# Kernel tuning notes

Measured on AMD Instinct MI355X. Metric: run time of the kernel, lower is better.

## Reference

```python
import jax, jax.numpy as jnp
import numpy as np
from jax import lax

DIM = 64           # LHMSA dim
C3 = 3 * DIM       # high-band channels
HEADS = C3 // 32   # 6
WS = 8             # window size
SHIFT = 4          # shift size
EPS = 1e-6


def _ln_chw(x, w, b):
    # channel-last layer norm applied to BCHW input over C
    xt = x.transpose(0, 2, 3, 1)
    mu = xt.mean(-1, keepdims=True)
    var = ((xt - mu) ** 2).mean(-1, keepdims=True)
    y = (xt - mu) / jnp.sqrt(var + EPS) * w + b
    return y.transpose(0, 3, 1, 2)


def _conv1x1(x, w):
    # w: (out_c, in_c), no bias
    return jnp.einsum('bchw,oc->bohw', x, w)


def _dwconv3(x, w):
    # depthwise 3x3, w: (C,1,3,3)
    C = x.shape[1]
    return lax.conv_general_dilated(x, w, (1, 1), ((1, 1), (1, 1)),
                                    dimension_numbers=('NCHW', 'OIHW', 'NCHW'),
                                    feature_group_count=C)


def _gelu(x):
    return jax.nn.gelu(x, approximate=False)


def _dwt(x):
    x01 = x[:, :, 0::2, :] * 0.5
    x02 = x[:, :, 1::2, :] * 0.5
    x1 = x01[:, :, :, 0::2]; x2 = x02[:, :, :, 0::2]
    x3 = x01[:, :, :, 1::2]; x4 = x02[:, :, :, 1::2]
    ll = x1 + x2 + x3 + x4
    high = jnp.concatenate([-x1 - x2 + x3 + x4,
                            -x1 + x2 - x3 + x4,
                            x1 - x2 - x3 + x4], axis=1)
    return ll, high


def _iwt(ll, high):
    B, C, H, W = ll.shape
    hl, lh, hh = jnp.split(high, 3, axis=1)
    x1 = (ll - hl - lh + hh) * 0.5
    x2 = (ll - hl + lh - hh) * 0.5
    x3 = (ll + hl - lh - hh) * 0.5
    x4 = (ll + hl + lh + hh) * 0.5
    even = jnp.stack([x1, x3], axis=-1).reshape(B, C, H, 2 * W)  # rows 0::2
    odd = jnp.stack([x2, x4], axis=-1).reshape(B, C, H, 2 * W)   # rows 1::2
    return jnp.stack([even, odd], axis=-2).reshape(B, C, 2 * H, 2 * W)


def _swin_mhsa(x, qkv_w, qkv_b, proj_w, proj_b, rpb_table, rpi):
    # x: (B, C3, H, W); H,W divisible by WS -> no padding path
    B, C, H, W = x.shape
    dh = C // HEADS
    scale = dh ** (-0.5)
    xh = x.transpose(0, 2, 3, 1)                           # BHWC
    xh = jnp.roll(xh, (-SHIFT, -SHIFT), axis=(1, 2))
    nh, nw = H // WS, W // WS
    xw = xh.reshape(B, nh, WS, nw, WS, C).transpose(0, 1, 3, 2, 4, 5)
    xw = xw.reshape(B * nh * nw, WS * WS, C)               # (nW, N, C)
    qkv = xw @ qkv_w.T + qkv_b                             # (nW, N, 3C)
    qkv = qkv.reshape(-1, WS * WS, 3, HEADS, dh).transpose(2, 0, 3, 1, 4)
    q, k, v = qkv[0], qkv[1], qkv[2]                       # (nW, h, N, dh)
    attn = jnp.einsum('whnd,whmd->whnm', q, k) * scale
    bias = rpb_table[rpi.reshape(-1)].reshape(WS * WS, WS * WS, HEADS)
    attn = jax.nn.softmax(attn + bias.transpose(2, 0, 1)[None], axis=-1)
    out = jnp.einsum('whnm,whmd->whnd', attn, v)
    out = out.transpose(0, 2, 1, 3).reshape(-1, WS * WS, C)
    out = out.reshape(B, nh, nw, WS, WS, C).transpose(0, 1, 3, 2, 4, 5)
    out = out.reshape(B, H, W, C)
    out = jnp.roll(out, (SHIFT, SHIFT), axis=(1, 2))
    out = out @ proj_w.T + proj_b
    return out.transpose(0, 3, 1, 2)


def _rel_pos_index():
    coords = np.stack(np.meshgrid(np.arange(WS), np.arange(WS), indexing='ij'))
    cf = coords.reshape(2, -1)
    rel = (cf[:, :, None] - cf[:, None, :]).transpose(1, 2, 0).astype(np.int64)
    rel[:, :, 0] += WS - 1
    rel[:, :, 1] += WS - 1
    rel[:, :, 0] *= 2 * WS - 1
    return rel.sum(-1)


def setup_inputs() -> dict:
    key = jax.random.key(0)
    ks = jax.random.split(key, 12)
    B, H, W = 2, 512, 512
    x = jax.random.normal(ks[0], (B, DIM, H, W), jnp.float32)
    s = 0.02
    inp = {
        'x': x,
        'norm_w': jnp.ones((C3,), jnp.float32),
        'norm_b': jnp.zeros((C3,), jnp.float32),
        'qkv_w': jax.random.normal(ks[1], (3 * C3, C3), jnp.float32) * s,
        'qkv_b': jnp.zeros((3 * C3,), jnp.float32),
        'proj_w': jax.random.normal(ks[2], (C3, C3), jnp.float32) * s,
        'proj_b': jnp.zeros((C3,), jnp.float32),
        'rpb_table': jax.random.normal(ks[3], ((2 * WS - 1) ** 2, HEADS), jnp.float32) * s,
        'aux_dw_w': jax.random.normal(ks[4], (DIM, 1, 3, 3), jnp.float32) * 0.1,
        'aux_pw_w': jax.random.normal(ks[5], (DIM, DIM), jnp.float32) * s,
        'cg1_w': jax.random.normal(ks[6], (C3 * 3 // 12, DIM), jnp.float32) * s,
        'cg2_w': jax.random.normal(ks[7], (C3, C3 * 3 // 12), jnp.float32) * s,
        'po_w': jax.random.normal(ks[8], (DIM, DIM), jnp.float32) * s,
        'gamma_main': jnp.full((1,), 1e-4, jnp.float32),
        'gamma_aux': jnp.full((1,), 0.5, jnp.float32),
        'gamma_cross': jnp.full((1,), 1e-5, jnp.float32),
        'rel_pos_index': jnp.asarray(_rel_pos_index(), jnp.int32),
    }
    return inp


def reference(x, norm_w, norm_b, qkv_w, qkv_b, proj_w, proj_b, rpb_table,
              aux_dw_w, aux_pw_w, cg1_w, cg2_w, po_w,
              gamma_main, gamma_aux, gamma_cross, rel_pos_index):
    ll, high = _dwt(x)
    high_norm = _ln_chw(high, norm_w, norm_b)
    refined_high = high + gamma_main * _swin_mhsa(high_norm, qkv_w, qkv_b,
                                                  proj_w, proj_b, rpb_table,
                                                  rel_pos_index)
    refined_ll = ll + gamma_aux * _conv1x1(_gelu(_dwconv3(ll, aux_dw_w)), aux_pw_w)
    gap = ll.mean((2, 3), keepdims=True)
    cross = jax.nn.sigmoid(_conv1x1(_gelu(_conv1x1(gap, cg1_w)), cg2_w))
    refined_high = refined_high * (1.0 + gamma_cross * (cross - 0.5) * 2.0)
    out = _iwt(refined_ll, refined_high)
    return _conv1x1(out - x, po_w)
```

## Files before the change

kernel.cpp:

```cpp
#include <hip/hip_runtime.h>
#include <hip/hip_bf16.h>
#include <math.h>

typedef __hip_bfloat16 bf16;
typedef short s8v __attribute__((ext_vector_type(8)));
typedef float f4v __attribute__((ext_vector_type(4)));
#define MFMA16(a,b,c) __builtin_amdgcn_mfma_f32_16x16x32_bf16(a,b,c,0,0,0)

#define B2   2
#define C64  64
#define C3   192
#define HEADS 6
#define NWIN 2048

#define P_NORMW 0
#define P_NORMB 192
#define P_QKVW  384
#define P_QKVB  110976
#define P_PROJW 111552
#define P_PROJB 148416
#define P_RPB   148608
#define P_AUXDW 149958
#define P_AUXPW 150534
#define P_CG1   154630
#define P_CG2   157702
#define P_PO    166918
#define P_GM    171014
#define P_GA    171015
#define P_GC    171016

#define WS_FLAG   0
#define WS_PARAMS 256
#define WS_GAP    684544
#define WS_AMUL   685568
#define WS_CVAL   687616
#define WS_TSTAT  689664
#define WS_LL     1738240
#define WS_DLLW   18515456
#define WS_WOUT   35292672
#define WS_HRAW   85624320
#define WS_WQKV   135955968
#define WS_WPROJ  136177152
#define WS_WPW    136250880
#define WS_WPO    136259072
#define WS_S12    136267264
#define WS_BIAS6  136271872

__device__ __forceinline__ float bfu(unsigned short u){
  return __uint_as_float(((unsigned)u) << 16);
}
__device__ __forceinline__ float LDR(const void* p, long i, bool isf){
  return isf ? ((const float*)p)[i] : bfu(((const unsigned short*)p)[i]);
}
template<bool ISF>
__device__ __forceinline__ float4 LD4(const void* p, long i){
  if constexpr (ISF) return *(const float4*)((const float*)p + i);
  else {
    const ushort4 u = *(const ushort4*)((const bf16*)p + i);
    float4 r; r.x = bfu(u.x); r.y = bfu(u.y); r.z = bfu(u.z); r.w = bfu(u.w);
    return r;
  }
}
template<bool ISF>
__device__ __forceinline__ void ST(void* p, long i, float v){
  if constexpr (ISF) ((float*)p)[i] = v;
  else ((bf16*)p)[i] = __float2bfloat16(v);
}
__device__ __forceinline__ float gelu_f(float x){
  const float z = 0.7978845608028654f * (x + 0.044715f * x*x*x);
  const float t = 1.f - 2.f / (__expf(2.f*z) + 1.f);
  return 0.5f * x * (1.f + t);
}
__device__ __forceinline__ unsigned pk2(float a, float b){
  return (unsigned)__bfloat16_as_ushort(__float2bfloat16(a)) |
         ((unsigned)__bfloat16_as_ushort(__float2bfloat16(b)) << 16);
}
__device__ __forceinline__ uint4 pk8(const float* v){
  uint4 r;
  r.x = pk2(v[0], v[1]); r.y = pk2(v[2], v[3]);
  r.z = pk2(v[4], v[5]); r.w = pk2(v[6], v[7]);
  return r;
}
__device__ __forceinline__ void gld16(const void* g, void* l){
  __builtin_amdgcn_global_load_lds(
      (const __attribute__((address_space(1))) void*)g,
      (__attribute__((address_space(3))) void*)l, 16, 0, 0);
}

__global__ __launch_bounds__(256) void detect_kernel(const void* x, int* flag){
  __shared__ int wildcnt;
  if (threadIdx.x == 0) wildcnt = 0;
  __syncthreads();
  const unsigned short* u = (const unsigned short*)x;
  int wild = 0;
  for (int i = threadIdx.x; i < 2048; i += 256){
    unsigned int v = ((unsigned int)u[i]) << 16;
    float f = __uint_as_float(v);
    float a = fabsf(f);
    if (!(a < 1e8f) || (a > 0.f && a < 1e-8f)) wild++;
  }
  atomicAdd(&wildcnt, wild);
  __syncthreads();
  if (threadIdx.x == 0) *flag = (wildcnt > 100) ? 1 : 0;
}

struct PP { const void* src[15]; float* dst[15]; int n[15]; };
__device__ void kprep_body(int vblk, const PP& pp, bool isf, const int* rpi,
                           bf16* wqkvF, bf16* wproj, bf16* wpw,
                           bf16* wpo, float* bias6T, float2* s12p){
  const int gid = vblk*256 + threadIdx.x;
  const int gsz = 512*256;
#pragma unroll
  for (int q = 0; q < 15; q++){
    const int n = pp.n[q];
    const void* s = pp.src[q];
    float* d = pp.dst[q];
    for (int i = gid; i < n; i += gsz) d[i] = LDR(s, i, isf);
  }
  const void* qkvw = pp.src[2];
  const void* normw = pp.src[0];
  for (int i = gid; i < 110592; i += gsz)
    wqkvF[i] = __float2bfloat16(LDR(qkvw, i, isf) * LDR(normw, i % 192, isf));
  for (int i = gid; i < 36864; i += gsz)
    wproj[i] = __float2bfloat16(LDR(pp.src[4], i, isf));
  for (int i = gid; i < 4096; i += gsz){
    wpw[i] = __float2bfloat16(LDR(pp.src[8], i, isf));
    wpo[i] = __float2bfloat16(LDR(pp.src[11], i, isf));
  }
  for (int j = gid; j < 24576; j += gsz){
    const int hh = j >> 12, nm = j & 4095;
    const int row = nm >> 6, col = nm & 63;
    bias6T[hh*4096 + col*64 + row] = LDR(pp.src[6], rpi[nm]*6 + hh, isf);
  }
  const int o = gid >> 4, lane = gid & 15;
  if (o < 576){
    float s1 = 0.f, s2 = 0.f;
    for (int c = lane; c < 192; c += 16){
      const float w = LDR(qkvw, o*192 + c, isf);
      s1 += w * LDR(normw, c, isf);
      s2 += w * LDR(pp.src[1], c, isf);
    }
    s1 += __shfl_xor(s1,1,16); s1 += __shfl_xor(s1,2,16);
    s1 += __shfl_xor(s1,4,16); s1 += __shfl_xor(s1,8,16);
    s2 += __shfl_xor(s2,1,16); s2 += __shfl_xor(s2,2,16);
    s2 += __shfl_xor(s2,4,16); s2 += __shfl_xor(s2,8,16);
    if (lane == 0){
      float2 v; v.x = s1; v.y = s2 + LDR(pp.src[3], o, isf);
      s12p[o] = v;
    }
  }
}

template<bool ISF>
__device__ void k1f_body(int wid, const void* xv, bf16* llb, bf16* hraw, float2* tstat){
  const int b  = wid >> 10;
  const int wh = (wid >> 5) & 31;
  const int ww = wid & 31;
  const int tid = threadIdx.x;
  const int tp = tid >> 3, l8 = tid & 7;
  const int t0 = tp*2;
  const int wi = t0 >> 3, wj0 = t0 & 7;
  const int h2 = (wh*8 + wi + 4) & 255;
  const int w2 = (ww*8 + wj0 + 4) & 255;
  const long rowbase = ((long)(2*h2) << 9) + 2*w2;
  float r0[3][8], r1[3][8];
  float s0 = 0.f, q0 = 0.f, s1 = 0.f, q1 = 0.f;
#pragma unroll
  for (int cc = 0; cc < 8; ++cc){
    const int c = l8*8 + cc;
    const long base = ((long)(b*64 + c) << 18) + rowbase;
    const float4 ta = LD4<ISF>(xv, base);
    const float4 tb = LD4<ISF>(xv, base + 512);
    float a = ta.x, cr = ta.y, bb = tb.x, dd = tb.y;
    const float ll0 = 0.5f*(a + bb + cr + dd);
    const float h00 = 0.5f*(-a - bb + cr + dd);
    const float h10 = 0.5f*(-a + bb - cr + dd);
    const float h20 = 0.5f*( a - bb - cr + dd);
    r0[0][cc] = h00; r0[1][cc] = h10; r0[2][cc] = h20;
    s0 += h00 + h10 + h20; q0 += h00*h00 + h10*h10 + h20*h20;
    a = ta.z; cr = ta.w; bb = tb.z; dd = tb.w;
    const float ll1 = 0.5f*(a + bb + cr + dd);
    const float h01 = 0.5f*(-a - bb + cr + dd);
    const float h11 = 0.5f*(-a + bb - cr + dd);
    const float h21 = 0.5f*( a - bb - cr + dd);
    r1[0][cc] = h01; r1[1][cc] = h11; r1[2][cc] = h21;
    s1 += h01 + h11 + h21; q1 += h01*h01 + h11*h11 + h21*h21;
    *(unsigned*)(llb + ((long)(b*64 + c) << 16) + ((long)h2 << 8) + w2) = pk2(ll0, ll1);
  }
  const long hb = ((long)wid*64 + t0)*192 + l8*8;
  *(uint4*)(hraw + hb)            = pk8(r0[0]);
  *(uint4*)(hraw + hb + 64)       = pk8(r0[1]);
  *(uint4*)(hraw + hb + 128)      = pk8(r0[2]);
  *(uint4*)(hraw + hb + 192)      = pk8(r1[0]);
  *(uint4*)(hraw + hb + 192 + 64) = pk8(r1[1]);
  *(uint4*)(hraw + hb + 192 +128) = pk8(r1[2]);
  s0 += __shfl_xor(s0,1,8); s0 += __shfl_xor(s0,2,8); s0 += __shfl_xor(s0,4,8);
  q0 += __shfl_xor(q0,1,8); q0 += __shfl_xor(q0,2,8); q0 += __shfl_xor(q0,4,8);
  s1 += __shfl_xor(s1,1,8); s1 += __shfl_xor(s1,2,8); s1 += __shfl_xor(s1,4,8);
  q1 += __shfl_xor(q1,1,8); q1 += __shfl_xor(q1,2,8); q1 += __shfl_xor(q1,4,8);
  if (l8 == 0){
    float mean = s0 * (1.f/192.f);
    float var = fmaxf(q0 * (1.f/192.f) - mean*mean, 0.f);
    float rstd = rsqrtf(var + 1e-6f);
    float2 st; st.x = rstd; st.y = mean * rstd;
    tstat[wid*64 + t0] = st;
    mean = s1 * (1.f/192.f);
    var = fmaxf(q1 * (1.f/192.f) - mean*mean, 0.f);
    rstd = rsqrtf(var + 1e-6f);
    st.x = rstd; st.y = mean * rstd;
    tstat[wid*64 + t0 + 1] = st;
  }
}

__global__ __launch_bounds__(256,4) void k1p(const void* xv, bf16* llb, bf16* hraw,
                                             float2* tstat, const int* flag, PP pp,
                                             const int* rpi, bf16* wqkvF, bf16* wproj,
                                             bf16* wpw, bf16* wpo, float* bias6T,
                                             float2* s12p){
  const bool isf = (*flag) != 0;
  const int blk = blockIdx.x;
  if (blk < NWIN){
    if (isf) k1f_body<true>(blk, xv, llb, hraw, tstat);
    else     k1f_body<false>(blk, xv, llb, hraw, tstat);
  } else {
    kprep_body(blk - NWIN, pp, isf, rpi, wqkvF, wproj, wpw, wpo, bias6T, s12p);
  }
}

__global__ __launch_bounds__(256) void k3_cross(const float* pf, const float* gap,
                                                float* amul, float* cval){
  __shared__ float t1[B2][48];
  __shared__ float g[B2][64];
  const int tid = threadIdx.x;
  if (tid < 128) g[tid >> 6][tid & 63] = gap[tid];
  __syncthreads();
  if (tid < 96){
    const int b = tid / 48, j = tid % 48;
    float s = 0.f;
    const float* w = pf + P_CG1 + j * 64;
    for (int c = 0; c < 64; ++c) s += w[c] * g[b][c];
    t1[b][j] = gelu_f(s);
  }
  __syncthreads();
  const float gm = pf[P_GM], gc = pf[P_GC];
  for (int o = tid; o < B2 * C3; o += 256){
    const int b = o / C3, ch = o % C3;
    float s = 0.f;
    const float* w = pf + P_CG2 + ch * 48;
    for (int j = 0; j < 48; ++j) s += w[j] * t1[b][j];
    const float cr = 1.f / (1.f + expf(-s));
    const float c = gc * (cr - 0.5f) * 2.f;
    cval[o] = c;
    amul[o] = gm * (1.f + c);
  }
}

__device__ void k4_body(char* sm, int g, const bf16* hraw, const float2* tstat,
                        const bf16* wqkvF, const float2* s12p, const float* bias6T,
                        bf16* wout){
  bf16* bstage = (bf16*)sm;
  const int xcd = g & 7, slot = g >> 3;
  const int pair = (slot/6)*8 + xcd;
  const int h    = slot - (slot/6)*6;
  const int tid = threadIdx.x;
  const int wv5 = tid >> 6;
  const int lw  = wv5 >> 2;
  const int rg  = wv5 & 3;
  const int l = tid & 63, lr = l & 15, lg = l >> 4;
  const int wid = pair*2 + lw;
  char* reg = sm + 36864 + lw*13312;
  bf16* bq = (bf16*)reg;
  bf16* bk = (bf16*)(reg + 4608);
  char* vtb = reg + 9216;
  bf16* bp = (bf16*)reg;
  const f4v fz = {0.f,0.f,0.f,0.f};
  const float scale = 0.17677669529663687f;
  const bf16* at = hraw + (long)wid * 12288;

#pragma unroll
  for (int pass = 0; pass < 5; ++pass){
    if (pass*512 + wv5*64 < 2304){
      const int idx = pass*512 + tid;
      const int rl  = idx / 24;
      const int off = (idx - rl*24) * 16;
      const int soff = off ^ ((rl & 7) << 4);
      const int grow = (rl >> 5)*192 + h*32 + (rl & 31);
      gld16(wqkvF + grow*192 + (soff >> 1),
            (char*)bstage + (pass*512 + wv5*64)*16);
    }
  }
  s8v aA[6];
#pragma unroll
  for (int ks = 0; ks < 6; ++ks)
    aA[ks] = *(const s8v*)(at + (rg*16+lr)*192 + ks*32 + lg*8);
  float2 st4[4];
#pragma unroll
  for (int i = 0; i < 4; ++i)
    st4[i] = tstat[wid*64 + rg*16 + lg*4 + i];
  __syncthreads();

  f4v acc[6];
#pragma unroll
  for (int nt = 0; nt < 6; ++nt) acc[nt] = fz;
#pragma unroll
  for (int ks = 0; ks < 6; ++ks){
    const int kb = (ks*32 + lg*8) * 2;
#pragma unroll
    for (int nt = 0; nt < 6; ++nt){
      const int row = nt*16 + lr;
      const s8v bfr = *(const s8v*)((const char*)bstage + row*384 + (kb ^ ((row&7)<<4)));
      acc[nt] = MFMA16(aA[ks], bfr, acc[nt]);
    }
  }
#pragma unroll
  for (int nt = 0; nt < 6; ++nt){
    const int ol = nt*16 + lr;
    const int p = ol >> 5, c = ol & 31;
    const int ocol = p*192 + h*32 + c;
    const float2 sp = s12p[ocol];
#pragma unroll
    for (int i = 0; i < 4; ++i){
      const int row = rg*16 + lg*4 + i;
      const float v = st4[i].x*acc[nt][i] - st4[i].y*sp.x + sp.y;
      if (p == 0)      bq[row*36 + c] = __float2bfloat16(v*scale);
      else if (p == 1) bk[row*36 + c] = __float2bfloat16(v);
      else             *(bf16*)(vtb + ((c*128 + row*2) ^ ((c&7)<<4))) = __float2bfloat16(v);
    }
  }
  __syncthreads();

  f4v bld[4];
#pragma unroll
  for (int nt = 0; nt < 4; ++nt)
    bld[nt] = *(const f4v*)(bias6T + h*4096 + (nt*16+lr)*64 + rg*16 + lg*4);
  f4v sacc[4];
  {
    const s8v a = *(const s8v*)(bq + (rg*16+lr)*36 + lg*8);
#pragma unroll
    for (int nt = 0; nt < 4; ++nt){
      const s8v bfr = *(const s8v*)(bk + (nt*16+lr)*36 + lg*8);
      sacc[nt] = MFMA16(a, bfr, bld[nt]);
    }
  }
  float pvv[4][4];
  float inv4[4];
#pragma unroll
  for (int i = 0; i < 4; ++i){
    float s = 0.f;
#pragma unroll
    for (int nt = 0; nt < 4; ++nt){
      const float e = __expf(sacc[nt][i]);
      pvv[i][nt] = e;
      s += e;
    }
    s += __shfl_xor(s, 1, 16);
    s += __shfl_xor(s, 2, 16);
    s += __shfl_xor(s, 4, 16);
    s += __shfl_xor(s, 8, 16);
    inv4[i] = 1.f/s;
  }
  __syncthreads();

#pragma unroll
  for (int i = 0; i < 4; ++i){
    const int row = rg*16 + lg*4 + i;
#pragma unroll
    for (int nt = 0; nt < 4; ++nt)
      bp[row*72 + nt*16 + lr] = __float2bfloat16(pvv[i][nt]);
  }
  f4v oacc[2] = {fz, fz};
#pragma unroll
  for (int ks2 = 0; ks2 < 2; ++ks2){
    const s8v a = *(const s8v*)(bp + (rg*16+lr)*72 + ks2*32 + lg*8);
#pragma unroll
    for (int nn = 0; nn < 2; ++nn){
      const int d = nn*16 + lr;
      const s8v bfr = *(const s8v*)(vtb + ((d*128 + (ks2*32+lg*8)*2) ^ ((d&7)<<4)));
      oacc[nn] = MFMA16(a, bfr, oacc[nn]);
    }
  }
#pragma unroll
  for (int nn = 0; nn < 2; ++nn)
#pragma unroll
    for (int i = 0; i < 4; ++i){
      const int row = rg*16 + lg*4 + i;
      wout[((long)wid*64 + row)*192 + h*32 + nn*16 + lr] =
        __float2bfloat16(oacc[nn][i] * inv4[i]);
    }
}

__device__ void k6f_body(char* smb, int blk6, const bf16* llb, const float* pf,
                         const bf16* wpw, bf16* dllw){
  const int tid = threadIdx.x;
  const int sub = tid >> 8;
  const int t2 = tid & 255;
  char* sm6 = smb + sub*24576;
  bf16* tile = (bf16*)sm6;
  bf16* t    = (bf16*)(sm6 + 15360);
  const int tl = blk6*2 + sub;
  const int b = tl >> 10, ti = (tl >> 5) & 31, tj = tl & 31;
  const int y0 = ti*8 - 1;
  const int x0 = tj*8 - 2;

  for (int e = t2; e < 7680; e += 256){
    const int col = e % 12;
    const int rc  = e / 12;
    const int row = rc % 10, ch = rc / 10;
    const int x = x0 + col, y = y0 + row;
    bf16 v = __float2bfloat16(0.f);
    if ((unsigned)x < 256u && (unsigned)y < 256u)
      v = llb[((long)(b*64 + ch) << 16) + ((long)y << 8) + x];
    tile[rc*12 + col] = v;
  }
  __syncthreads();

  {
    const int tok = t2 & 63, cgrp = t2 >> 6;
    const int iy = tok >> 3, ix = tok & 7;
#pragma unroll
    for (int cc = 0; cc < 16; ++cc){
      const int c = cgrp*16 + cc;
      const float* wk = pf + P_AUXDW + c*9;
      float s = 0.f;
#pragma unroll
      for (int ky = 0; ky < 3; ++ky)
#pragma unroll
        for (int kx = 0; kx < 3; ++kx)
          s += wk[ky*3 + kx] * __bfloat162float(tile[(c*10 + iy + ky)*12 + ix + 1 + kx]);
      t[tok*72 + c] = __float2bfloat16(gelu_f(s));
    }
  }
  __syncthreads();

  const int wv = t2 >> 6, l = t2 & 63, lr = l & 15, lg = l >> 4;
  const f4v fz = {0.f,0.f,0.f,0.f};
  f4v acc[4];
#pragma unroll
  for (int nt = 0; nt < 4; ++nt) acc[nt] = fz;
#pragma unroll
  for (int ks = 0; ks < 2; ++ks){
    const s8v a = *(const s8v*)(t + (wv*16+lr)*72 + ks*32 + lg*8);
#pragma unroll
    for (int nt = 0; nt < 4; ++nt){
      const s8v bfr = *(const s8v*)(wpw + (nt*16+lr)*64 + ks*32 + lg*8);
      acc[nt] = MFMA16(a, bfr, acc[nt]);
    }
  }
  const float ga = pf[P_GA];
#pragma unroll
  for (int i = 0; i < 4; ++i){
    const int p = wv*16 + lg*4 + i;
    const int y = ti*8 + (p >> 3), x = tj*8 + (p & 7);
    const int sy = (y - 4) & 255, sx = (x - 4) & 255;
    const int wd = b*1024 + (sy >> 3)*32 + (sx >> 3);
    const int tok2 = (sy & 7)*8 + (sx & 7);
    const long ob = ((long)wd*64 + tok2)*64;
#pragma unroll
    for (int nt = 0; nt < 4; ++nt)
      dllw[ob + nt*16 + lr] = __float2bfloat16(ga * acc[nt][i]);
  }
}

__device__ void k2_body(char* smb, int bc, const bf16* llb, float* gap){
  float* red = (float*)smb;
  const int tid = threadIdx.x;
  const uint4* p = (const uint4*)(llb + ((long)bc << 16));
  float s = 0.f;
  for (int i = tid; i < 8192; i += 512){
    const uint4 v = p[i];
    s += __uint_as_float(v.x << 16) + __uint_as_float(v.x & 0xffff0000u);
    s += __uint_as_float(v.y << 16) + __uint_as_float(v.y & 0xffff0000u);
    s += __uint_as_float(v.z << 16) + __uint_as_float(v.z & 0xffff0000u);
    s += __uint_as_float(v.w << 16) + __uint_as_float(v.w & 0xffff0000u);
  }
  red[tid] = s; __syncthreads();
  for (int st = 256; st > 0; st >>= 1){
    if (tid < st) red[tid] += red[tid + st];
    __syncthreads();
  }
  if (tid == 0) gap[bc] = red[0] * (1.f / 65536.f);
}

__global__ __launch_bounds__(512,4) void kmix(const bf16* hraw, const float2* tstat,
                                              const bf16* wqkvF, const float2* s12p,
                                              const float* bias6T, bf16* wout,
                                              const bf16* llb, const float* pf,
                                              const bf16* wpw, bf16* dllw, float* gap){
  __shared__ __align__(16) char sm[63488];
  const int blk = blockIdx.x;
  if (blk < 7168){
    const int g7 = blk / 7, r7 = blk - g7*7;
    if (r7 < 6) k4_body(sm, g7*6 + r7, hraw, tstat, wqkvF, s12p, bias6T, wout);
    else        k6f_body(sm, g7, llb, pf, wpw, dllw);
  } else {
    k2_body(sm, blk - 7168, llb, gap);
  }
}

__global__ __launch_bounds__(256,5) void k5_proj(bf16* wout, const bf16* hraw,
                                                 const bf16* wproj, const float* pf,
                                                 const float* amul, const float* cval){
  __shared__ __align__(16) bf16 bufC[64*192];
  const int wid = blockIdx.x;
  const int b  = wid >> 10;
  const int tid = threadIdx.x;
  const int wv = tid >> 6, l = tid & 63, lr = l & 15, lg = l >> 4;

  {
    const bf16* hsrc = hraw + (long)wid * 12288;
#pragma unroll
    for (int pass = 0; pass < 6; ++pass){
      const int idx = pass*256 + tid;
      const int row = idx / 24;
      const int off = (idx % 24) * 16;
      const int soff = off ^ ((row & 7) << 4);
      gld16(hsrc + row*192 + (soff >> 1),
            (char*)bufC + (pass*256 + wv*64)*16);
    }
  }

  const f4v fz = {0.f,0.f,0.f,0.f};
  const bf16* at = wout + (long)wid * 12288;

  f4v acc[3][4];
#pragma unroll
  for (int nt = 0; nt < 3; ++nt)
#pragma unroll
    for (int mt = 0; mt < 4; ++mt) acc[nt][mt] = fz;
#pragma unroll
  for (int ks = 0; ks < 6; ++ks){
    const int k0 = ks*32;
    s8v a[4];
#pragma unroll
    for (int mt = 0; mt < 4; ++mt)
      a[mt] = *(const s8v*)(at + (mt*16+lr)*192 + k0 + lg*8);
#pragma unroll
    for (int nt = 0; nt < 3; ++nt){
      const int ocol = (wv*3+nt)*16 + lr;
      const s8v bfr = *(const s8v*)(wproj + ocol*192 + k0 + lg*8);
#pragma unroll
      for (int mt = 0; mt < 4; ++mt) acc[nt][mt] = MFMA16(a[mt], bfr, acc[nt][mt]);
    }
  }
  __syncthreads();
#pragma unroll
  for (int nt = 0; nt < 3; ++nt){
    const int col = (wv*3+nt)*16 + lr;
    const int bc = b*192 + col;
    const float am = amul[bc], cv = cval[bc], pb = pf[P_PROJB + col];
#pragma unroll
    for (int mt = 0; mt < 4; ++mt)
#pragma unroll
      for (int i = 0; i < 4; ++i){
        const int row = mt*16 + lg*4 + i;
        const float hv = __bfloat162float(
          *(const bf16*)((const char*)bufC + row*384 + ((col*2) ^ ((row&7)<<4))));
        wout[(long)wid*12288 + row*192 + col] =
          __float2bfloat16(am*(acc[nt][mt][i] + pb) + cv*hv);
      }
  }
}

template<bool ISF>
__device__ void k7_body(const bf16* dvalw, const bf16* dllw, const bf16* wpo,
                        void* out, char* yp){
  const int blk = blockIdx.x;
  const int b = blk >> 10, hh = (blk >> 1) & 511, half = blk & 1;
  const int h2 = hh >> 1, posH = hh & 1;
  const int th = (h2 + 252) & 255;
  const int wh = th >> 3, wi = th & 7;
  const int tid = threadIdx.x;
  const int j = tid & 7;
#pragma unroll
  for (int pass = 0; pass < 8; ++pass){
    const int p = pass*32 + (tid >> 3);
    const int ww2 = half*256 + p;
    const int w2 = ww2 >> 1, posW = ww2 & 1;
    const int tw = (w2 + 252) & 255;
    const int ww = tw >> 3, wj = tw & 7;
    const int wid = b*1024 + wh*32 + ww;
    const int tok = wi*8 + wj;
    const long dvb = ((long)wid*64 + tok)*192 + j*8;
    const s8v hl8 = *(const s8v*)(dvalw + dvb);
    const s8v lh8 = *(const s8v*)(dvalw + dvb + 64);
    const s8v hh8 = *(const s8v*)(dvalw + dvb + 128);
    const s8v dl8 = *(const s8v*)(dllw + ((long)wid*64 + tok)*64 + j*8);
    const float s1 = posW ? 0.5f : -0.5f;
    const float s2 = posH ? 0.5f : -0.5f;
    const float s3 = posW == posH ? 0.5f : -0.5f;
    float e[8];
#pragma unroll
    for (int q = 0; q < 8; ++q)
      e[q] = 0.5f*bfu((unsigned short)dl8[q]) + s1*bfu((unsigned short)hl8[q])
           + s2*bfu((unsigned short)lh8[q]) + s3*bfu((unsigned short)hh8[q]);
    *(uint4*)(yp + ((p*128 + j*16) ^ ((p&7)<<4))) = pk8(e);
  }
  __syncthreads();
  const int wv = tid >> 6, l = tid & 63, lr = l & 15, lg = l >> 4;
  const f4v fz = {0.f,0.f,0.f,0.f};
  f4v acc[4][4];
#pragma unroll
  for (int mt = 0; mt < 4; ++mt)
#pragma unroll
    for (int nt = 0; nt < 4; ++nt) acc[mt][nt] = fz;
#pragma unroll
  for (int ks = 0; ks < 2; ++ks){
    const int k0 = ks*32;
    s8v a[4];
#pragma unroll
    for (int mt = 0; mt < 4; ++mt)
      a[mt] = *(const s8v*)(wpo + (mt*16+lr)*64 + k0 + lg*8);
#pragma unroll
    for (int nt = 0; nt < 4; ++nt){
      const int prow = wv*64 + nt*16 + lr;
      const s8v bfr = *(const s8v*)(yp + ((prow*128 + (k0+lg*8)*2) ^ ((prow&7)<<4)));
#pragma unroll
      for (int mt = 0; mt < 4; ++mt) acc[mt][nt] = MFMA16(a[mt], bfr, acc[mt][nt]);
    }
  }
  const int px0 = half*256 + wv*64;
#pragma unroll
  for (int mt = 0; mt < 4; ++mt)
#pragma unroll
    for (int nt = 0; nt < 4; ++nt)
#pragma unroll
      for (int i = 0; i < 4; ++i){
        const int c = mt*16 + lg*4 + i;
        const long ob = ((long)(b*64 + c)*512 + hh)*512 + px0 + nt*16 + lr;
        ST<ISF>(out, ob, acc[mt][nt][i]);
      }
}
__global__ __launch_bounds__(256,4) void k7_out(const bf16* dvalw, const bf16* dllw,
                                                const bf16* wpo, void* out, const int* flag){
  __shared__ __align__(16) char yp[32768];
  if (*flag) k7_body<true>(dvalw, dllw, wpo, out, yp);
  else       k7_body<false>(dvalw, dllw, wpo, out, yp);
}

extern "C" void kernel_launch(void* const* d_in, const int* in_sizes, int n_in,
                              void* d_out, int out_size, void* d_ws, size_t ws_size,
                              hipStream_t stream){
  char* ws = (char*)d_ws;
  int*   flag = (int*)(ws + WS_FLAG);
  float* pf   = (float*)(ws + WS_PARAMS);
  float* gap  = (float*)(ws + WS_GAP);
  float* amul = (float*)(ws + WS_AMUL);
  float* cval = (float*)(ws + WS_CVAL);
  float2* tstat=(float2*)(ws + WS_TSTAT);
  bf16*  llb  = (bf16*)(ws + WS_LL);
  bf16*  dllw = (bf16*)(ws + WS_DLLW);
  bf16*  wout = (bf16*)(ws + WS_WOUT);
  bf16*  hraw = (bf16*)(ws + WS_HRAW);
  bf16*  wqkvF= (bf16*)(ws + WS_WQKV);
  bf16*  wproj= (bf16*)(ws + WS_WPROJ);
  bf16*  wpw  = (bf16*)(ws + WS_WPW);
  bf16*  wpo  = (bf16*)(ws + WS_WPO);
  float2* s12p= (float2*)(ws + WS_S12);
  float* bias6= (float*)(ws + WS_BIAS6);
  const int* rpi = (const int*)d_in[16];

  detect_kernel<<<1, 256, 0, stream>>>(d_in[0], flag);

  PP pp;
  const int pidx[15] = {1,2,3,4,5,6,7,8,9,10,11,12,13,14,15};
  const int poff[15] = {P_NORMW,P_NORMB,P_QKVW,P_QKVB,P_PROJW,P_PROJB,P_RPB,
                        P_AUXDW,P_AUXPW,P_CG1,P_CG2,P_PO,P_GM,P_GA,P_GC};
  for (int q = 0; q < 15; q++){
    pp.src[q] = d_in[pidx[q]];
    pp.dst[q] = pf + poff[q];
    pp.n[q]   = in_sizes[pidx[q]];
  }

  k1p    <<<NWIN + 512, 256, 0, stream>>>(d_in[0], llb, hraw, tstat, flag, pp, rpi,
                                          wqkvF, wproj, wpw, wpo, bias6, s12p);
  kmix   <<<7296, 512, 0, stream>>>(hraw, tstat, wqkvF, s12p, bias6, wout,
                                    llb, pf, wpw, dllw, gap);
  k3_cross<<<1,   256, 0, stream>>>(pf, gap, amul, cval);
  k5_proj<<<NWIN, 256, 0, stream>>>(wout, hraw, wproj, pf, amul, cval);
  k7_out <<<2048, 256, 0, stream>>>(wout, dllw, wpo, d_out, flag);
}
```

Baseline: 379.0 us.

## Fold cross-gate MLP into proj kernel, batch DWT loads, raise MFMA priority

Removes the single-block k3_cross launch. Each k5_proj block now recomputes the small cross-gate MLP from gap into shared memory, which is redundant work repeated across 2048 blocks but saves a launch and a serial one-block stage. The DWT loop in k1 now issues four channel loads before computing on them, to get more memory-level parallelism. s_setprio is raised around the MFMA loops in the attention kernel.

```diff
diff --git a/kernel.cpp b/kernel.cpp
--- a/kernel.cpp
+++ b/kernel.cpp
@@ -32,8 +32,6 @@
 #define WS_FLAG   0
 #define WS_PARAMS 256
 #define WS_GAP    684544
-#define WS_AMUL   685568
-#define WS_CVAL   687616
 #define WS_TSTAT  689664
 #define WS_LL     1738240
 #define WS_DLLW   18515456
@@ -166,26 +164,35 @@
   float r0[3][8], r1[3][8];
   float s0 = 0.f, q0 = 0.f, s1 = 0.f, q1 = 0.f;
 #pragma unroll
-  for (int cc = 0; cc < 8; ++cc){
-    const int c = l8*8 + cc;
-    const long base = ((long)(b*64 + c) << 18) + rowbase;
-    const float4 ta = LD4<ISF>(xv, base);
-    const float4 tb = LD4<ISF>(xv, base + 512);
-    float a = ta.x, cr = ta.y, bb = tb.x, dd = tb.y;
-    const float ll0 = 0.5f*(a + bb + cr + dd);
-    const float h00 = 0.5f*(-a - bb + cr + dd);
-    const float h10 = 0.5f*(-a + bb - cr + dd);
-    const float h20 = 0.5f*( a - bb - cr + dd);
-    r0[0][cc] = h00; r0[1][cc] = h10; r0[2][cc] = h20;
-    s0 += h00 + h10 + h20; q0 += h00*h00 + h10*h10 + h20*h20;
-    a = ta.z; cr = ta.w; bb = tb.z; dd = tb.w;
-    const float ll1 = 0.5f*(a + bb + cr + dd);
-    const float h01 = 0.5f*(-a - bb + cr + dd);
-    const float h11 = 0.5f*(-a + bb - cr + dd);
-    const float h21 = 0.5f*( a - bb - cr + dd);
-    r1[0][cc] = h01; r1[1][cc] = h11; r1[2][cc] = h21;
-    s1 += h01 + h11 + h21; q1 += h01*h01 + h11*h11 + h21*h21;
-    *(unsigned*)(llb + ((long)(b*64 + c) << 16) + ((long)h2 << 8) + w2) = pk2(ll0, ll1);
+  for (int g4 = 0; g4 < 2; ++g4){
+    float4 ta[4], tb[4];
+#pragma unroll
+    for (int u = 0; u < 4; ++u){
+      const int c = l8*8 + g4*4 + u;
+      const long base = ((long)(b*64 + c) << 18) + rowbase;
+      ta[u] = LD4<ISF>(xv, base);
+      tb[u] = LD4<ISF>(xv, base + 512);
+    }
+#pragma unroll
+    for (int u = 0; u < 4; ++u){
+      const int cc = g4*4 + u;
+      const int c = l8*8 + cc;
+      float a = ta[u].x, cr = ta[u].y, bb = tb[u].x, dd = tb[u].y;
+      const float ll0 = 0.5f*(a + bb + cr + dd);
+      const float h00 = 0.5f*(-a - bb + cr + dd);
+      const float h10 = 0.5f*(-a + bb - cr + dd);
+      const float h20 = 0.5f*( a - bb - cr + dd);
+      r0[0][cc] = h00; r0[1][cc] = h10; r0[2][cc] = h20;
+      s0 += h00 + h10 + h20; q0 += h00*h00 + h10*h10 + h20*h20;
+      a = ta[u].z; cr = ta[u].w; bb = tb[u].z; dd = tb[u].w;
+      const float ll1 = 0.5f*(a + bb + cr + dd);
+      const float h01 = 0.5f*(-a - bb + cr + dd);
+      const float h11 = 0.5f*(-a + bb - cr + dd);
+      const float h21 = 0.5f*( a - bb - cr + dd);
+      r1[0][cc] = h01; r1[1][cc] = h11; r1[2][cc] = h21;
+      s1 += h01 + h11 + h21; q1 += h01*h01 + h11*h11 + h21*h21;
+      *(unsigned*)(llb + ((long)(b*64 + c) << 16) + ((long)h2 << 8) + w2) = pk2(ll0, ll1);
+    }
   }
   const long hb = ((long)wid*64 + t0)*192 + l8*8;
   *(uint4*)(hraw + hb)            = pk8(r0[0]);
@@ -227,34 +234,6 @@
   }
 }
 
-__global__ __launch_bounds__(256) void k3_cross(const float* pf, const float* gap,
-                                                float* amul, float* cval){
-  __shared__ float t1[B2][48];
-  __shared__ float g[B2][64];
-  const int tid = threadIdx.x;
-  if (tid < 128) g[tid >> 6][tid & 63] = gap[tid];
-  __syncthreads();
-  if (tid < 96){
-    const int b = tid / 48, j = tid % 48;
-    float s = 0.f;
-    const float* w = pf + P_CG1 + j * 64;
-    for (int c = 0; c < 64; ++c) s += w[c] * g[b][c];
-    t1[b][j] = gelu_f(s);
-  }
-  __syncthreads();
-  const float gm = pf[P_GM], gc = pf[P_GC];
-  for (int o = tid; o < B2 * C3; o += 256){
-    const int b = o / C3, ch = o % C3;
-    float s = 0.f;
-    const float* w = pf + P_CG2 + ch * 48;
-    for (int j = 0; j < 48; ++j) s += w[j] * t1[b][j];
-    const float cr = 1.f / (1.f + expf(-s));
-    const float c = gc * (cr - 0.5f) * 2.f;
-    cval[o] = c;
-    amul[o] = gm * (1.f + c);
-  }
-}
-
 __device__ void k4_body(char* sm, int g, const bf16* hraw, const float2* tstat,
                         const bf16* wqkvF, const float2* s12p, const float* bias6T,
                         bf16* wout){
@@ -302,6 +281,7 @@
   f4v acc[6];
 #pragma unroll
   for (int nt = 0; nt < 6; ++nt) acc[nt] = fz;
+  __builtin_amdgcn_s_setprio(1);
 #pragma unroll
   for (int ks = 0; ks < 6; ++ks){
     const int kb = (ks*32 + lg*8) * 2;
@@ -312,6 +292,7 @@
       acc[nt] = MFMA16(aA[ks], bfr, acc[nt]);
     }
   }
+  __builtin_amdgcn_s_setprio(0);
 #pragma unroll
   for (int nt = 0; nt < 6; ++nt){
     const int ol = nt*16 + lr;
@@ -369,6 +350,7 @@
       bp[row*72 + nt*16 + lr] = __float2bfloat16(pvv[i][nt]);
   }
   f4v oacc[2] = {fz, fz};
+  __builtin_amdgcn_s_setprio(1);
 #pragma unroll
   for (int ks2 = 0; ks2 < 2; ++ks2){
     const s8v a = *(const s8v*)(bp + (rg*16+lr)*72 + ks2*32 + lg*8);
@@ -379,6 +361,7 @@
       oacc[nn] = MFMA16(a, bfr, oacc[nn]);
     }
   }
+  __builtin_amdgcn_s_setprio(0);
 #pragma unroll
   for (int nn = 0; nn < 2; ++nn)
 #pragma unroll
@@ -499,8 +482,10 @@
 
 __global__ __launch_bounds__(256,5) void k5_proj(bf16* wout, const bf16* hraw,
                                                  const bf16* wproj, const float* pf,
-                                                 const float* amul, const float* cval){
+                                                 const float* gap){
   __shared__ __align__(16) bf16 bufC[64*192];
+  __shared__ float t1s[48];
+  __shared__ float amL[192], cvL[192];
   const int wid = blockIdx.x;
   const int b  = wid >> 10;
   const int tid = threadIdx.x;
@@ -519,6 +504,23 @@
     }
   }
 
+  if (tid < 48){
+    float s = 0.f;
+    const float* w = pf + P_CG1 + tid*64;
+    for (int c = 0; c < 64; ++c) s += w[c] * gap[b*64 + c];
+    t1s[tid] = gelu_f(s);
+  }
+  __syncthreads();
+  if (tid < 192){
+    float s = 0.f;
+    const float* w = pf + P_CG2 + tid*48;
+    for (int j = 0; j < 48; ++j) s += w[j] * t1s[j];
+    const float cr = 1.f / (1.f + __expf(-s));
+    const float cc = pf[P_GC] * (cr - 0.5f) * 2.f;
+    cvL[tid] = cc;
+    amL[tid] = pf[P_GM] * (1.f + cc);
+  }
+
   const f4v fz = {0.f,0.f,0.f,0.f};
   const bf16* at = wout + (long)wid * 12288;
 
@@ -546,8 +548,7 @@
 #pragma unroll
   for (int nt = 0; nt < 3; ++nt){
     const int col = (wv*3+nt)*16 + lr;
-    const int bc = b*192 + col;
-    const float am = amul[bc], cv = cval[bc], pb = pf[P_PROJB + col];
+    const float am = amL[col], cv = cvL[col], pb = pf[P_PROJB + col];
 #pragma unroll
     for (int mt = 0; mt < 4; ++mt)
 #pragma unroll
@@ -644,8 +645,6 @@
   int*   flag = (int*)(ws + WS_FLAG);
   float* pf   = (float*)(ws + WS_PARAMS);
   float* gap  = (float*)(ws + WS_GAP);
-  float* amul = (float*)(ws + WS_AMUL);
-  float* cval = (float*)(ws + WS_CVAL);
   float2* tstat=(float2*)(ws + WS_TSTAT);
   bf16*  llb  = (bf16*)(ws + WS_LL);
   bf16*  dllw = (bf16*)(ws + WS_DLLW);
@@ -675,7 +674,6 @@
                                           wqkvF, wproj, wpw, wpo, bias6, s12p);
   kmix   <<<7296, 512, 0, stream>>>(hraw, tstat, wqkvF, s12p, bias6, wout,
                                     llb, pf, wpw, dllw, gap);
-  k3_cross<<<1,   256, 0, stream>>>(pf, gap, amul, cval);
-  k5_proj<<<NWIN, 256, 0, stream>>>(wout, hraw, wproj, pf, amul, cval);
+  k5_proj<<<NWIN, 256, 0, stream>>>(wout, hraw, wproj, pf, gap);
   k7_out <<<2048, 256, 0, stream>>>(wout, dllw, wpo, d_out, flag);
 }
```

After: 380.1 us, median of 2. About the same (+0.3%).
